# Kernel tuning notes

Measured on AMD Instinct MI355X. Metric: run time of the kernel, lower is better.

The kernel has to match this reference:

```python
import jax, jax.numpy as jnp
import numpy as np

B, S, D_MODEL, H, BLOCK = 2, 4096, 1024, 16, 512
HEAD = D_MODEL // H  # 64


def setup_inputs() -> dict:
    key = jax.random.key(0)
    ks = jax.random.split(key, 5)
    w_scale = 1.0 / np.sqrt(D_MODEL)  # variance_scaling(1.0,'fan_in','normal')-like magnitude
    return {
        "inputs_q": jax.random.normal(ks[0], (B, S, D_MODEL), jnp.float32),
        "Wq": jax.random.normal(ks[1], (D_MODEL, D_MODEL), jnp.float32) * w_scale,
        "bq": jnp.zeros((D_MODEL,), jnp.float32),
        "Wk": jax.random.normal(ks[2], (D_MODEL, D_MODEL), jnp.float32) * w_scale,
        "bk": jnp.zeros((D_MODEL,), jnp.float32),
        "Wv": jax.random.normal(ks[3], (D_MODEL, D_MODEL), jnp.float32) * w_scale,
        "bv": jnp.zeros((D_MODEL,), jnp.float32),
        "Wo": jax.random.normal(ks[4], (D_MODEL, D_MODEL), jnp.float32) * w_scale,
        "bo": jnp.zeros((D_MODEL,), jnp.float32),
    }


def _flash_attention(q, k, v):
    """Blocked online-softmax attention. q,k,v: [B,S,H,D] -> [B,S,H,D].

    Scans over KV blocks of size BLOCK, maintaining running max (m),
    running sum of exp (l), and unnormalized output (o), exactly matching
    the original module's blocked accumulation math (no mask/bias/dropout).
    """
    scale = 1.0 / jnp.sqrt(jnp.asarray(HEAD, q.dtype))
    n_kv_blocks = S // BLOCK
    # [n_blocks, B, BLOCK, H, D]
    kb = k.reshape(B, n_kv_blocks, BLOCK, H, HEAD).transpose(1, 0, 2, 3, 4)
    vb = v.reshape(B, n_kv_blocks, BLOCK, H, HEAD).transpose(1, 0, 2, 3, 4)

    o0 = jnp.zeros_like(q)                                   # [B,S,H,D]
    m0 = jnp.full((B, S, H), -jnp.inf, dtype=q.dtype)        # running max
    l0 = jnp.zeros((B, S, H), dtype=q.dtype)                 # running sum-exp

    def step(carry, kv):
        o, m, l = carry
        k_blk, v_blk = kv
        # [B,H,S,BLOCK] scores for all queries vs this kv block
        scores = jnp.einsum('bqhd,bkhd->bhqk', q, k_blk) * scale
        blk_max = jnp.max(scores, axis=-1).transpose(0, 2, 1)   # [B,S,H]
        new_m = jnp.maximum(m, blk_max)
        alpha = jnp.exp(m - new_m)                               # rescale old stats
        p = jnp.exp(scores - new_m.transpose(0, 2, 1)[..., None])
        new_l = alpha * l + jnp.sum(p, axis=-1).transpose(0, 2, 1)
        new_o = o * alpha[..., None] + jnp.einsum('bhqk,bkhd->bqhd', p, v_blk)
        return (new_o, new_m, new_l), None

    (o, m, l), _ = jax.lax.scan(step, (o0, m0, l0), (kb, vb))
    return o / l[..., None]


def reference(inputs_q, Wq, bq, Wk, bk, Wv, bv, Wo, bo):
    q = (inputs_q @ Wq + bq).reshape(B, S, H, HEAD)
    k = (inputs_q @ Wk + bk).reshape(B, S, H, HEAD)  # self-attention: k=v=q input
    v = (inputs_q @ Wv + bv).reshape(B, S, H, HEAD)
    x = _flash_attention(q, k, v).reshape(B, S, D_MODEL)
    return x @ Wo + bo
```

## Files before the change

kernel.cpp:

```cpp
#include <hip/hip_runtime.h>
#include <hip/hip_bf16.h>
#include <stdint.h>

#define B_ 2
#define S_ 4096
#define DM 1024
#define H_ 16
#define HD 64
#define M_TOT (B_*S_)

typedef unsigned short u16;
typedef short s16x8 __attribute__((ext_vector_type(8)));
typedef short s16x4 __attribute__((ext_vector_type(4)));
typedef float f32x4 __attribute__((ext_vector_type(4)));
typedef uint32_t u32x2 __attribute__((ext_vector_type(2)));

#if __has_builtin(__builtin_amdgcn_mfma_f32_16x16x16_bf16)
#define MFMA16(A,B,C) __builtin_amdgcn_mfma_f32_16x16x16_bf16(A,B,C,0,0,0)
#elif __has_builtin(__builtin_amdgcn_mfma_f32_16x16x16bf16_1k)
#define MFMA16(A,B,C) __builtin_amdgcn_mfma_f32_16x16x16bf16_1k(A,B,C,0,0,0)
#else
static __device__ __forceinline__ f32x4 mfma16_asm(s16x4 a, s16x4 b, f32x4 c){
  f32x4 d;
  asm volatile("v_mfma_f32_16x16x16_bf16 %0, %1, %2, %3" : "=v"(d) : "v"(a), "v"(b), "v"(c));
  return d;
}
#define MFMA16(A,B,C) mfma16_asm(A,B,C)
#endif

__device__ __forceinline__ u16 f2bf(float f){
  union { float fv; uint32_t u; } x; x.fv = f;
  uint32_t r = (x.u + 0x7fffu + ((x.u >> 16) & 1u)) >> 16;
  return (u16)r;
}

#if __has_builtin(__builtin_amdgcn_cvt_pk_bf16_f32)
typedef __bf16 bf16x2_t __attribute__((ext_vector_type(2)));
__device__ __forceinline__ uint32_t pkbf(float a, float b){
  union { bf16x2_t v; uint32_t u; } x;
  x.v = __builtin_amdgcn_cvt_pk_bf16_f32(a, b);
  return x.u;
}
#else
__device__ __forceinline__ uint32_t pkbf(float a, float b){
  union { float f; uint32_t u; } xa, xb; xa.f = a; xb.f = b;
  return __builtin_amdgcn_perm(xb.u + 0x8000u, xa.u + 0x8000u, 0x07060302u);
}
#endif

__device__ __forceinline__ void gld_lds16(const void* g, void* l){
  __builtin_amdgcn_global_load_lds((const __attribute__((address_space(1))) void*)g,
                                   (__attribute__((address_space(3))) void*)l, 16, 0, 0);
}

__global__ __launch_bounds__(256) void k_cvt_x(const float* __restrict__ x, u16* __restrict__ xb){
  size_t i = (size_t)blockIdx.x * 256 + threadIdx.x;
  const float4* p = (const float4*)x + i*2;
  float4 a = p[0], b = p[1];
  union { u16 u[8]; uint4 v; } o;
  o.u[0]=f2bf(a.x); o.u[1]=f2bf(a.y); o.u[2]=f2bf(a.z); o.u[3]=f2bf(a.w);
  o.u[4]=f2bf(b.x); o.u[5]=f2bf(b.y); o.u[6]=f2bf(b.z); o.u[7]=f2bf(b.w);
  ((uint4*)xb)[i] = o.v;
}

__global__ __launch_bounds__(256) void k_wt(const float* __restrict__ W0, const float* __restrict__ W1,
                                            const float* __restrict__ W2, const float* __restrict__ W3,
                                            u16* __restrict__ wt){
  const float* W = blockIdx.z==0?W0: blockIdx.z==1?W1: blockIdx.z==2?W2:W3;
  u16* out = wt + (size_t)blockIdx.z * DM * DM;
  int n0 = blockIdx.x*64, k0 = blockIdx.y*64;
  __shared__ u16 T[64*66];
  int t = threadIdx.x;
  #pragma unroll
  for (int i=0;i<4;i++){
    int idx = t + i*256;
    int kr = idx >> 4, n4 = idx & 15;
    float4 v = *(const float4*)(W + (size_t)(k0+kr)*DM + n0 + n4*4);
    T[(n4*4+0)*66 + kr] = f2bf(v.x);
    T[(n4*4+1)*66 + kr] = f2bf(v.y);
    T[(n4*4+2)*66 + kr] = f2bf(v.z);
    T[(n4*4+3)*66 + kr] = f2bf(v.w);
  }
  __syncthreads();
  #pragma unroll
  for (int i=0;i<2;i++){
    int idx = t + i*256;
    int n = idx >> 3, k8 = idx & 7;
    union { u16 u[8]; uint4 v; } o;
    #pragma unroll
    for (int j=0;j<8;j++) o.u[j] = T[n*66 + k8*8 + j];
    *(uint4*)(out + (size_t)(n0+n)*DM + k0 + k8*8) = o.v;
  }
}

__device__ __forceinline__ void gemm128(const u16* __restrict__ A, const u16* __restrict__ BT,
                                        const float* __restrict__ bias, float scale,
                                        u16* __restrict__ outb, float* __restrict__ outf,
                                        int m0, int n0){
  __shared__ __align__(16) u16 As[128*32];
  __shared__ __align__(16) u16 Bs[128*32];
  int t = threadIdx.x;
  int lane = t & 63, w = t >> 6;
  int wm = w & 1, wn = w >> 1;
  int c16 = lane & 15, quad = lane >> 4;
  f32x4 acc[4][4] = {};
  for (int k0 = 0; k0 < DM; k0 += 32){
    #pragma unroll
    for (int i=0;i<2;i++){
      int idx = t + i*256;
      int row = idx >> 2, c8 = (idx & 3) << 3;
      gld_lds16(A  + (size_t)(m0+row)*DM + k0 + c8, &As[idx*8]);
      gld_lds16(BT + (size_t)(n0+row)*DM + k0 + c8, &Bs[idx*8]);
    }
    __syncthreads();
    s16x8 af[4], bf[4];
    #pragma unroll
    for (int mi=0;mi<4;mi++) af[mi] = *(const s16x8*)&As[(wm*64+mi*16+c16)*32 + quad*8];
    #pragma unroll
    for (int ni=0;ni<4;ni++) bf[ni] = *(const s16x8*)&Bs[(wn*64+ni*16+c16)*32 + quad*8];
    #pragma unroll
    for (int mi=0;mi<4;mi++)
      #pragma unroll
      for (int ni=0;ni<4;ni++)
        acc[mi][ni] = __builtin_amdgcn_mfma_f32_16x16x32_bf16(af[mi], bf[ni], acc[mi][ni], 0, 0, 0);
    __syncthreads();
  }
  #pragma unroll
  for (int mi=0;mi<4;mi++){
    #pragma unroll
    for (int ni=0;ni<4;ni++){
      int col = n0 + wn*64 + ni*16 + c16;
      float bc = bias[col];
      #pragma unroll
      for (int r=0;r<4;r++){
        int row = m0 + wm*64 + mi*16 + quad*4 + r;
        float v = (acc[mi][ni][r] + bc) * scale;
        if (outb) outb[(size_t)row*DM + col] = f2bf(v);
        else      outf[(size_t)row*DM + col] = v;
      }
    }
  }
}

#define CL2 0.18033688011112042f

__device__ __forceinline__ void gemm_swz(int wg, int& m0, int& n0){
  int xcd = wg & 7, loc = wg >> 3;
  m0 = ((xcd << 3) + (loc >> 3)) * 128;
  n0 = (loc & 7) * 128;
}

__global__ __launch_bounds__(256) void k_gemm_qkv(const u16* __restrict__ xb, const u16* __restrict__ wt,
                                                  const float* __restrict__ b0, const float* __restrict__ b1,
                                                  const float* __restrict__ b2,
                                                  u16* __restrict__ q, u16* __restrict__ k, u16* __restrict__ v){
  int z = blockIdx.z;
  const u16* BT = wt + (size_t)z*DM*DM;
  const float* bias = z==0?b0: z==1?b1:b2;
  u16* out = z==0?q: z==1?k:v;
  float scale = (z==0) ? CL2 : 1.0f;
  int m0, n0;
  gemm_swz(blockIdx.x + (blockIdx.y << 3), m0, n0);
  gemm128(xb, BT, bias, scale, out, nullptr, m0, n0);
}

__global__ __launch_bounds__(256) void k_gemm_out(const u16* __restrict__ ab, const u16* __restrict__ wto,
                                                  const float* __restrict__ bias, float* __restrict__ out){
  int m0, n0;
  gemm_swz(blockIdx.x + (blockIdx.y << 3), m0, n0);
  gemm128(ab, wto, bias, 1.0f, nullptr, out, m0, n0);
}

__global__ __launch_bounds__(256) void k_vt(const u16* __restrict__ vb, u16* __restrict__ vt){
  __shared__ u16 T[64*66];
  int s0 = blockIdx.x*64, h = blockIdx.y, b = blockIdx.z;
  int t = threadIdx.x;
  #pragma unroll
  for (int i=0;i<2;i++){
    int idx = t + i*256;
    int sr = idx >> 3, d8 = idx & 7;
    s16x8 v = *(const s16x8*)(vb + ((size_t)(b*S_ + s0 + sr))*DM + h*64 + d8*8);
    #pragma unroll
    for (int j=0;j<8;j++) T[(d8*8+j)*66 + sr] = ((const u16*)&v)[j];
  }
  __syncthreads();
  #pragma unroll
  for (int i=0;i<2;i++){
    int idx = t + i*256;
    int d = idx >> 3, s8 = idx & 7;
    union { u16 u[8]; uint4 v; } o;
    #pragma unroll
    for (int j=0;j<8;j++) o.u[j] = T[d*66 + s8*8 + j];
    *(uint4*)(vt + ((size_t)((b*H_ + h)*64 + d))*S_ + s0 + s8*8) = o.v;
  }
}

__global__ __launch_bounds__(512, 2) void k_attn(const u16* __restrict__ qg, const u16* __restrict__ kg,
                                                 const u16* __restrict__ vtg, u16* __restrict__ ao){
  __shared__ __align__(16) char smem[67584];
  float* Ob  = (float*)smem;
  u16*   ObT = (u16*)smem;
  float* Lb  = (float*)(smem + 65536);

  int t = threadIdx.x, lane = t & 63, w = t >> 6;
  int c16 = lane & 15, quad = lane >> 4;
  int qq = w & 3, kh = w >> 2;
  int wg = blockIdx.x + (blockIdx.y << 4) + (blockIdx.z << 8);
  int xcd = wg & 7, loc = wg >> 3;
  int nw = (xcd << 6) + loc;
  int q0 = (nw & 15) * 256;
  int hb = nw >> 4;
  int h = hb & 15, b = hb >> 4;
  size_t rowbase = (size_t)b * S_;
  const u16* vbase = vtg + ((size_t)(b*H_ + h)) * 64 * S_;

  int krow0 = t >> 3,         ksw0 = ((t & 7) ^ (krow0 & 7));
  int krow1 = (t + 512) >> 3, ksw1 = ((t & 7) ^ (krow1 & 7));
  const u16* kgp0 = kg + (rowbase + krow0)*DM + h*64 + ksw0*8;
  const u16* kgp1 = kg + (rowbase + krow1)*DM + h*64 + ksw1*8;
  int vrow0 = t >> 4,         vsw0 = ((t & 15) ^ (vrow0 & 15));
  int vrow1 = (t + 512) >> 4, vsw1 = ((t & 15) ^ (vrow1 & 15));
  const u16* vgp0 = vbase + (size_t)vrow0*S_ + vsw0*8;
  const u16* vgp1 = vbase + (size_t)vrow1*S_ + vsw1*8;
  char* kd0 = smem + t*16;
  char* kd1 = smem + t*16 + 8192;
  char* vd0 = smem + 16384 + t*16;
  char* vd1 = smem + 16384 + t*16 + 8192;

  auto stage = [&](int boff, int kv0){
    size_t ko = (size_t)kv0 * DM;
    gld_lds16(kgp0 + ko, kd0 + boff);
    gld_lds16(kgp1 + ko, kd1 + boff);
    gld_lds16(vgp0 + kv0, vd0 + boff);
    gld_lds16(vgp1 + kv0, vd1 + boff);
  };

  stage(0, 0);

  s16x8 qf[4][2];
  #pragma unroll
  for (int nt=0;nt<4;nt++)
    #pragma unroll
    for (int ks=0;ks<2;ks++)
      qf[nt][ks] = *(const s16x8*)(qg + (rowbase + q0 + qq*64 + nt*16 + c16)*DM + h*64 + ks*32 + quad*8);

  f32x4 oacc[4][4] = {};
  float lacc[4] = {0.f,0.f,0.f,0.f};

  auto compute = [&](int boff){
    const u16* Kt = (const u16*)(smem + boff);
    const u16* Vt = (const u16*)(smem + boff + 16384);

    f32x4 sc[4][4] = {};
    #pragma unroll
    for (int mt=0;mt<4;mt++){
      #pragma unroll
      for (int ks=0;ks<2;ks++){
        s16x8 kf = *(const s16x8*)&Kt[(kh*64 + mt*16 + c16)*64 + (((ks*4 + quad) ^ (c16 & 7)) * 8)];
        #pragma unroll
        for (int nt=0;nt<4;nt++)
          sc[mt][nt] = __builtin_amdgcn_mfma_f32_16x16x32_bf16(kf, qf[nt][ks], sc[mt][nt], 0,0,0);
      }
    }

    uint32_t pk[4][4][2];
    #pragma unroll
    for (int mt=0;mt<4;mt++){
      #pragma unroll
      for (int nt=0;nt<4;nt++){
        float p0 = __builtin_amdgcn_exp2f(sc[mt][nt][0]);
        float p1 = __builtin_amdgcn_exp2f(sc[mt][nt][1]);
        float p2 = __builtin_amdgcn_exp2f(sc[mt][nt][2]);
        float p3 = __builtin_amdgcn_exp2f(sc[mt][nt][3]);
        lacc[nt] += (p0 + p1) + (p2 + p3);
        pk[mt][nt][0] = pkbf(p0, p1);
        pk[mt][nt][1] = pkbf(p2, p3);
      }
    }

    #pragma unroll
    for (int mt=0;mt<4;mt++){
      #pragma unroll
      for (int dt=0;dt<4;dt++){
        s16x4 vf = *(const s16x4*)&Vt[(dt*16 + c16)*128 + (((kh*8 + mt*2 + (quad>>1)) ^ c16) * 8) + (quad & 1)*4];
        #pragma unroll
        for (int nt=0;nt<4;nt++){
          union { uint32_t u[2]; s16x4 v; } pp;
          pp.u[0] = pk[mt][nt][0]; pp.u[1] = pk[mt][nt][1];
          oacc[dt][nt] = MFMA16(vf, pp.v, oacc[dt][nt]);
        }
      }
    }
  };

  #define NT (S_/128)
  #pragma unroll 1
  for (int kvt = 0; kvt < NT-1; ++kvt){
    stage(((kvt+1) & 1) * 32768, (kvt+1)*128);
    asm volatile("s_waitcnt vmcnt(4)" ::: "memory");
    __builtin_amdgcn_s_barrier();
    __builtin_amdgcn_sched_barrier(0);
    compute((kvt & 1) * 32768);
    __builtin_amdgcn_s_barrier();
    __builtin_amdgcn_sched_barrier(0);
  }
  asm volatile("s_waitcnt vmcnt(0)" ::: "memory");
  __builtin_amdgcn_s_barrier();
  __builtin_amdgcn_sched_barrier(0);
  compute(((NT-1) & 1) * 32768);

  float lw[4];
  #pragma unroll
  for (int nt=0;nt<4;nt++){
    float l = lacc[nt];
    l += __shfl_xor(l, 16);
    l += __shfl_xor(l, 32);
    lw[nt] = l;
  }
  __syncthreads();
  if (quad == 0){
    #pragma unroll
    for (int nt=0;nt<4;nt++) Lb[kh*256 + qq*64 + nt*16 + c16] = lw[nt];
  }
  uint32_t pko[4][4][2];
  float invl[4];
  #pragma unroll
  for (int dh=0; dh<2; dh++){
    if (kh == 1){
      #pragma unroll
      for (int dt2=0;dt2<2;dt2++)
        #pragma unroll
        for (int nt=0;nt<4;nt++)
          *(f32x4*)&Ob[(qq*64 + nt*16 + c16)*36 + dt2*16 + quad*4] = oacc[dh*2+dt2][nt];
    }
    __syncthreads();
    if (kh == 0){
      if (dh == 0){
        #pragma unroll
        for (int nt=0;nt<4;nt++){
          int ql = qq*64 + nt*16 + c16;
          invl[nt] = 1.0f / (Lb[ql] + Lb[256 + ql]);
        }
      }
      #pragma unroll
      for (int dt2=0;dt2<2;dt2++)
        #pragma unroll
        for (int nt=0;nt<4;nt++){
          f32x4 p = *(const f32x4*)&Ob[(qq*64 + nt*16 + c16)*36 + dt2*16 + quad*4];
          f32x4 o = oacc[dh*2+dt2][nt] + p;
          pko[dh*2+dt2][nt][0] = pkbf(o[0]*invl[nt], o[1]*invl[nt]);
          pko[dh*2+dt2][nt][1] = pkbf(o[2]*invl[nt], o[3]*invl[nt]);
        }
    }
    __syncthreads();
  }
  if (kh == 0){
    #pragma unroll
    for (int dt=0;dt<4;dt++)
      #pragma unroll
      for (int nt=0;nt<4;nt++){
        u32x2 pr; pr.x = pko[dt][nt][0]; pr.y = pko[dt][nt][1];
        *(u32x2*)&ObT[(qq*64 + nt*16 + c16)*72 + dt*16 + quad*4] = pr;
      }
  }
  __syncthreads();
  #pragma unroll
  for (int i=0;i<4;i++){
    int idx = t + i*512;
    int qr = idx >> 3, qc = (idx & 7)*8;
    *(s16x8*)(ao + (rowbase + q0 + qr)*DM + h*64 + qc) = *(const s16x8*)&ObT[qr*72 + qc];
  }
}

extern "C" void kernel_launch(void* const* d_in, const int* in_sizes, int n_in,
                              void* d_out, int out_size, void* d_ws, size_t ws_size,
                              hipStream_t stream){
  const float* x  = (const float*)d_in[0];
  const float* Wq = (const float*)d_in[1];
  const float* bq = (const float*)d_in[2];
  const float* Wk = (const float*)d_in[3];
  const float* bk = (const float*)d_in[4];
  const float* Wv = (const float*)d_in[5];
  const float* bv = (const float*)d_in[6];
  const float* Wo = (const float*)d_in[7];
  const float* bo = (const float*)d_in[8];

  char* ws = (char*)d_ws;
  const size_t XB = (size_t)M_TOT*DM*2;
  const size_t WTB = (size_t)4*DM*DM*2;
  u16* xb  = (u16*)(ws);
  u16* wt  = (u16*)(ws + XB);
  u16* qb  = (u16*)(ws + XB + WTB);
  u16* kb  = (u16*)(ws + XB + WTB + XB);
  u16* vb  = (u16*)(ws + XB + WTB + 2*XB);
  u16* vtb = (u16*)(ws + XB + WTB + 3*XB);
  u16* aob = (u16*)(ws + XB + WTB + 4*XB);

  k_cvt_x<<<dim3((M_TOT*DM)/(256*8)), 256, 0, stream>>>(x, xb);
  k_wt<<<dim3(16,16,4), 256, 0, stream>>>(Wq, Wk, Wv, Wo, wt);
  k_gemm_qkv<<<dim3(8, M_TOT/128, 3), 256, 0, stream>>>(xb, wt, bq, bk, bv, qb, kb, vb);
  k_vt<<<dim3(S_/64, H_, B_), 256, 0, stream>>>(vb, vtb);
  k_attn<<<dim3(S_/256, H_, B_), 512, 0, stream>>>(qb, kb, vtb, aob);
  k_gemm_out<<<dim3(8, M_TOT/128), 256, 0, stream>>>(aob, wt + (size_t)3*DM*DM, bo, (float*)d_out);
}
```

Baseline: 343.8 us.

## Produce transposed V directly from the QKV GEMM and widen the GEMM K-tile with swizzle

The V projection is computed as W_v^T·X^T, so the GEMM writes V already transposed in a [head_dim, B*S] layout. This removes the separate transpose kernel and its extra read and write of V, and the attention kernel's V addressing is updated to match. Separately, the shared GEMM K-tile is widened from 32 to 64 with XOR-swizzled LDS addressing, which halves the barrier count and aims to reduce bank conflicts. The costs are more LDS per block and a strided row-bias store pattern in the transposed output path.

```diff
diff --git a/kernel.cpp b/kernel.cpp
--- a/kernel.cpp
+++ b/kernel.cpp
@@ -94,35 +94,51 @@
 }
 
 __device__ __forceinline__ void gemm128(const u16* __restrict__ A, const u16* __restrict__ BT,
-                                        const float* __restrict__ bias, float scale,
+                                        const float* __restrict__ bias, bool brow, float scale,
                                         u16* __restrict__ outb, float* __restrict__ outf,
-                                        int m0, int n0){
-  __shared__ __align__(16) u16 As[128*32];
-  __shared__ __align__(16) u16 Bs[128*32];
+                                        int m0, int n0, int ldo){
+  __shared__ __align__(16) u16 As[128*64];
+  __shared__ __align__(16) u16 Bs[128*64];
   int t = threadIdx.x;
   int lane = t & 63, w = t >> 6;
   int wm = w & 1, wn = w >> 1;
   int c16 = lane & 15, quad = lane >> 4;
   f32x4 acc[4][4] = {};
-  for (int k0 = 0; k0 < DM; k0 += 32){
-    #pragma unroll
-    for (int i=0;i<2;i++){
-      int idx = t + i*256;
-      int row = idx >> 2, c8 = (idx & 3) << 3;
-      gld_lds16(A  + (size_t)(m0+row)*DM + k0 + c8, &As[idx*8]);
-      gld_lds16(BT + (size_t)(n0+row)*DM + k0 + c8, &Bs[idx*8]);
+  const u16* ap[4]; const u16* bp[4];
+  #pragma unroll
+  for (int i=0;i<4;i++){
+    int c = t + i*256;
+    int row = c >> 3, scol = (c & 7) ^ (row & 7);
+    ap[i] = A  + (size_t)(m0+row)*DM + scol*8;
+    bp[i] = BT + (size_t)(n0+row)*DM + scol*8;
+  }
+  for (int k0 = 0; k0 < DM; k0 += 64){
+    #pragma unroll
+    for (int i=0;i<4;i++){
+      int c = t + i*256;
+      gld_lds16(ap[i] + k0, &As[c*8]);
+      gld_lds16(bp[i] + k0, &Bs[c*8]);
     }
     __syncthreads();
-    s16x8 af[4], bf[4];
-    #pragma unroll
-    for (int mi=0;mi<4;mi++) af[mi] = *(const s16x8*)&As[(wm*64+mi*16+c16)*32 + quad*8];
-    #pragma unroll
-    for (int ni=0;ni<4;ni++) bf[ni] = *(const s16x8*)&Bs[(wn*64+ni*16+c16)*32 + quad*8];
-    #pragma unroll
-    for (int mi=0;mi<4;mi++)
-      #pragma unroll
-      for (int ni=0;ni<4;ni++)
-        acc[mi][ni] = __builtin_amdgcn_mfma_f32_16x16x32_bf16(af[mi], bf[ni], acc[mi][ni], 0, 0, 0);
+    #pragma unroll
+    for (int ks=0; ks<2; ks++){
+      s16x8 af[4], bfr[4];
+      #pragma unroll
+      for (int mi=0;mi<4;mi++){
+        int row = wm*64 + mi*16 + c16;
+        af[mi] = *(const s16x8*)&As[row*64 + (((ks*4 + quad) ^ (row & 7))*8)];
+      }
+      #pragma unroll
+      for (int ni=0;ni<4;ni++){
+        int row = wn*64 + ni*16 + c16;
+        bfr[ni] = *(const s16x8*)&Bs[row*64 + (((ks*4 + quad) ^ (row & 7))*8)];
+      }
+      #pragma unroll
+      for (int mi=0;mi<4;mi++)
+        #pragma unroll
+        for (int ni=0;ni<4;ni++)
+          acc[mi][ni] = __builtin_amdgcn_mfma_f32_16x16x32_bf16(af[mi], bfr[ni], acc[mi][ni], 0, 0, 0);
+    }
     __syncthreads();
   }
   #pragma unroll
@@ -130,13 +146,14 @@
     #pragma unroll
     for (int ni=0;ni<4;ni++){
       int col = n0 + wn*64 + ni*16 + c16;
-      float bc = bias[col];
+      float bc = brow ? 0.0f : bias[col];
       #pragma unroll
       for (int r=0;r<4;r++){
         int row = m0 + wm*64 + mi*16 + quad*4 + r;
-        float v = (acc[mi][ni][r] + bc) * scale;
-        if (outb) outb[(size_t)row*DM + col] = f2bf(v);
-        else      outf[(size_t)row*DM + col] = v;
+        float bb = brow ? bias[row] : bc;
+        float v = (acc[mi][ni][r] + bb) * scale;
+        if (outb) outb[(size_t)row*ldo + col] = f2bf(v);
+        else      outf[(size_t)row*ldo + col] = v;
       }
     }
   }
@@ -153,46 +170,27 @@
 __global__ __launch_bounds__(256) void k_gemm_qkv(const u16* __restrict__ xb, const u16* __restrict__ wt,
                                                   const float* __restrict__ b0, const float* __restrict__ b1,
                                                   const float* __restrict__ b2,
-                                                  u16* __restrict__ q, u16* __restrict__ k, u16* __restrict__ v){
+                                                  u16* __restrict__ q, u16* __restrict__ k, u16* __restrict__ vt){
   int z = blockIdx.z;
-  const u16* BT = wt + (size_t)z*DM*DM;
-  const float* bias = z==0?b0: z==1?b1:b2;
-  u16* out = z==0?q: z==1?k:v;
-  float scale = (z==0) ? CL2 : 1.0f;
   int m0, n0;
   gemm_swz(blockIdx.x + (blockIdx.y << 3), m0, n0);
-  gemm128(xb, BT, bias, scale, out, nullptr, m0, n0);
+  const u16* Aarg; const u16* Barg; const float* bias; float scale; u16* out;
+  int mm, nn, ldo; bool brow;
+  if (z == 2){
+    Aarg = wt + 2*(size_t)DM*DM; Barg = xb; bias = b2; brow = true;  scale = 1.0f;
+    out = vt; mm = n0; nn = m0; ldo = M_TOT;
+  } else {
+    Aarg = xb; Barg = wt + (size_t)z*DM*DM; bias = z ? b1 : b0; brow = false;
+    scale = z ? 1.0f : CL2; out = z ? k : q; mm = m0; nn = n0; ldo = DM;
+  }
+  gemm128(Aarg, Barg, bias, brow, scale, out, nullptr, mm, nn, ldo);
 }
 
 __global__ __launch_bounds__(256) void k_gemm_out(const u16* __restrict__ ab, const u16* __restrict__ wto,
                                                   const float* __restrict__ bias, float* __restrict__ out){
   int m0, n0;
   gemm_swz(blockIdx.x + (blockIdx.y << 3), m0, n0);
-  gemm128(ab, wto, bias, 1.0f, nullptr, out, m0, n0);
-}
-
-__global__ __launch_bounds__(256) void k_vt(const u16* __restrict__ vb, u16* __restrict__ vt){
-  __shared__ u16 T[64*66];
-  int s0 = blockIdx.x*64, h = blockIdx.y, b = blockIdx.z;
-  int t = threadIdx.x;
-  #pragma unroll
-  for (int i=0;i<2;i++){
-    int idx = t + i*256;
-    int sr = idx >> 3, d8 = idx & 7;
-    s16x8 v = *(const s16x8*)(vb + ((size_t)(b*S_ + s0 + sr))*DM + h*64 + d8*8);
-    #pragma unroll
-    for (int j=0;j<8;j++) T[(d8*8+j)*66 + sr] = ((const u16*)&v)[j];
-  }
-  __syncthreads();
-  #pragma unroll
-  for (int i=0;i<2;i++){
-    int idx = t + i*256;
-    int d = idx >> 3, s8 = idx & 7;
-    union { u16 u[8]; uint4 v; } o;
-    #pragma unroll
-    for (int j=0;j<8;j++) o.u[j] = T[d*66 + s8*8 + j];
-    *(uint4*)(vt + ((size_t)((b*H_ + h)*64 + d))*S_ + s0 + s8*8) = o.v;
-  }
+  gemm128(ab, wto, bias, false, 1.0f, nullptr, out, m0, n0, DM);
 }
 
 __global__ __launch_bounds__(512, 2) void k_attn(const u16* __restrict__ qg, const u16* __restrict__ kg,
@@ -212,7 +210,7 @@
   int hb = nw >> 4;
   int h = hb & 15, b = hb >> 4;
   size_t rowbase = (size_t)b * S_;
-  const u16* vbase = vtg + ((size_t)(b*H_ + h)) * 64 * S_;
+  const u16* vbase = vtg + ((size_t)h*64)*M_TOT + b*S_;
 
   int krow0 = t >> 3,         ksw0 = ((t & 7) ^ (krow0 & 7));
   int krow1 = (t + 512) >> 3, ksw1 = ((t & 7) ^ (krow1 & 7));
@@ -220,8 +218,8 @@
   const u16* kgp1 = kg + (rowbase + krow1)*DM + h*64 + ksw1*8;
   int vrow0 = t >> 4,         vsw0 = ((t & 15) ^ (vrow0 & 15));
   int vrow1 = (t + 512) >> 4, vsw1 = ((t & 15) ^ (vrow1 & 15));
-  const u16* vgp0 = vbase + (size_t)vrow0*S_ + vsw0*8;
-  const u16* vgp1 = vbase + (size_t)vrow1*S_ + vsw1*8;
+  const u16* vgp0 = vbase + (size_t)vrow0*M_TOT + vsw0*8;
+  const u16* vgp1 = vbase + (size_t)vrow1*M_TOT + vsw1*8;
   char* kd0 = smem + t*16;
   char* kd1 = smem + t*16 + 8192;
   char* vd0 = smem + 16384 + t*16;
@@ -392,14 +390,12 @@
   u16* wt  = (u16*)(ws + XB);
   u16* qb  = (u16*)(ws + XB + WTB);
   u16* kb  = (u16*)(ws + XB + WTB + XB);
-  u16* vb  = (u16*)(ws + XB + WTB + 2*XB);
-  u16* vtb = (u16*)(ws + XB + WTB + 3*XB);
-  u16* aob = (u16*)(ws + XB + WTB + 4*XB);
+  u16* vtb = (u16*)(ws + XB + WTB + 2*XB);
+  u16* aob = (u16*)(ws + XB + WTB + 3*XB);
 
   k_cvt_x<<<dim3((M_TOT*DM)/(256*8)), 256, 0, stream>>>(x, xb);
   k_wt<<<dim3(16,16,4), 256, 0, stream>>>(Wq, Wk, Wv, Wo, wt);
-  k_gemm_qkv<<<dim3(8, M_TOT/128, 3), 256, 0, stream>>>(xb, wt, bq, bk, bv, qb, kb, vb);
-  k_vt<<<dim3(S_/64, H_, B_), 256, 0, stream>>>(vb, vtb);
+  k_gemm_qkv<<<dim3(8, M_TOT/128, 3), 256, 0, stream>>>(xb, wt, bq, bk, bv, qb, kb, vtb);
   k_attn<<<dim3(S_/256, H_, B_), 512, 0, stream>>>(qb, kb, vtb, aob);
   k_gemm_out<<<dim3(8, M_TOT/128), 256, 0, stream>>>(aob, wt + (size_t)3*DM*DM, bo, (float*)d_out);
 }
```

After: 349.3 us. Within noise of the previous version (+1.6%).
